# Performance work log

Hardware: AMD Instinct MI355X
Metric: run time of the kernel (lower is better)

Reference implementation:

```python
import jax, jax.numpy as jnp
import numpy as np

# --- quantization-format simulation helpers (numpy, used only in setup) ---
FP4_GRID = np.array([0.0, 0.5, 1.0, 1.5, 2.0, 3.0, 4.0, 6.0], np.float32)  # e2m1 magnitudes
FP4_MID = (FP4_GRID[:-1] + FP4_GRID[1:]) / 2.0
E4M3_MAX = 448.0


def _round_e4m3(x):
    """Round-to-nearest onto an fp8 e4m3-like grid (3 mantissa bits, clamp to 448)."""
    x = np.clip(x, -E4M3_MAX, E4M3_MAX)
    a = np.abs(x)
    e = np.clip(np.floor(np.log2(np.maximum(a, 1e-12))), -6, 8)
    step = np.exp2(e - 3)
    return (np.round(x / step) * step).astype(np.float32)


def _quant_fp4_mag(a):
    """Nearest e2m1 magnitude for non-negative a."""
    idx = np.searchsorted(FP4_MID, a)
    return FP4_GRID[idx]


def setup_inputs() -> dict:
    rng = np.random.default_rng(0)
    IN, OUT, P = 4096, 4096, 8
    k_fp8 = ((IN // P + 127) // 128) * 128   # 512
    k_fp4 = IN - k_fp8                       # 3584

    w = (rng.standard_normal((OUT, IN)) * 0.023).astype(np.float32)
    w4 = w[:, :k_fp4]
    w8 = w[:, k_fp4:]

    # --- NVFP4 quantization: per-128 fp32 outer scale, per-16 e4m3 inner scale ---
    b128 = w4.reshape(OUT, k_fp4 // 128, 128)
    os = np.maximum(np.abs(b128).max(-1) / (6.0 * E4M3_MAX), 1e-12).astype(np.float32)  # (OUT, k4/128)
    b16 = w4.reshape(OUT, k_fp4 // 128, 8, 16)
    is_q = _round_e4m3(np.abs(b16).max(-1) / 6.0 / os[..., None])  # (OUT, k4/128, 8)
    denom = np.maximum(is_q * os[..., None], 1e-12)
    q4 = np.sign(b16) * _quant_fp4_mag(np.abs(b16) / denom[..., None])
    w_q_fp4 = q4.reshape(OUT, k_fp4).astype(np.float32)
    w_is_fp4 = is_q.reshape(OUT, k_fp4 // 16).astype(np.float32)
    w_os_fp4 = os

    # --- fp8 quantization: per-32 e8m0 (power-of-2) scale ---
    b32 = w8.reshape(OUT, k_fp8 // 32, 32)
    amax = np.maximum(np.abs(b32).max(-1), 1e-12)
    s8 = np.exp2(np.ceil(np.log2(amax / E4M3_MAX))).astype(np.float32)
    w_q_fp8 = _round_e4m3(b32 / s8[..., None]).reshape(OUT, k_fp8)
    w_s_fp8 = s8

    # --- dequantized transposed weight buffer (as the module precomputes) ---
    w4_dq = w_q_fp4 * np.repeat(w_is_fp4, 16, 1) * np.repeat(w_os_fp4, 128, 1)
    w8_dq = w_q_fp8 * np.repeat(w_s_fp8, 32, 1)
    w_t = np.ascontiguousarray(np.concatenate([w4_dq, w8_dq], 1).T)  # (IN, OUT)

    x = rng.standard_normal((8192, IN)).astype(np.float32)
    return {
        "x": jnp.asarray(x),
        "w_q_fp4": jnp.asarray(w_q_fp4),
        "w_os_fp4": jnp.asarray(w_os_fp4),
        "w_is_fp4": jnp.asarray(w_is_fp4),
        "w_t": jnp.asarray(w_t),
        "w_q_fp8": jnp.asarray(w_q_fp8),
        "w_s_fp8": jnp.asarray(w_s_fp8),
    }


def reference(x, w_q_fp4, w_os_fp4, w_is_fp4, w_t, w_q_fp8, w_s_fp8):
    OUT = w_q_fp4.shape[0]
    k4 = w_q_fp4.shape[1]
    # fused dequant of fp4 partition: value * inner_scale(per 16) * outer_scale(per 128)
    w4 = (w_q_fp4.reshape(OUT, k4 // 16, 16) * w_is_fp4[..., None]).reshape(OUT, k4)
    w4 = (w4.reshape(OUT, k4 // 128, 128) * w_os_fp4[..., None]).reshape(OUT, k4)
    # dequant of fp8 partition: value * e8m0 scale (per 32)
    k8 = w_q_fp8.shape[1]
    w8 = (w_q_fp8.reshape(OUT, k8 // 32, 32) * w_s_fp8[..., None]).reshape(OUT, k8)
    W = jnp.concatenate([w4, w8], axis=1)  # (OUT, IN)
    return x @ W.T  # (tokens, OUT)
```

## Files before the change

kernel.cpp:

```cpp
#include <hip/hip_runtime.h>
#include <stdint.h>

#define K_DIM 4096
#define N_DIM 4096
#define KS_DIM (K_DIM / 32)
#define NT_DIM (N_DIM / 16)

typedef __attribute__((ext_vector_type(8))) short s16x8;
typedef __attribute__((ext_vector_type(4))) float f32x4;

static __device__ __forceinline__ unsigned short f32_to_bf16(float f) {
    union { float f; unsigned int u; } v; v.f = f;
    unsigned int u = v.u;
    u += 0x7FFFu + ((u >> 16) & 1u);
    return (unsigned short)(u >> 16);
}


extern "C" __global__ __launch_bounds__(256)
void pack_x_k(const float* __restrict__ in,
              unsigned short* __restrict__ out, int MT) {
    __shared__ __align__(16) unsigned short tile[16][1032];
    const int kc = blockIdx.x;
    const int mt = blockIdx.y;
    const int t = threadIdx.x;
#pragma unroll
    for (int r = 0; r < 16; ++r) {
        float4 v = *(const float4*)(in + (size_t)(mt * 16 + r) * K_DIM
                                    + kc * 1024 + t * 4);
        tile[r][t * 4 + 0] = f32_to_bf16(v.x);
        tile[r][t * 4 + 1] = f32_to_bf16(v.y);
        tile[r][t * 4 + 2] = f32_to_bf16(v.z);
        tile[r][t * 4 + 3] = f32_to_bf16(v.w);
    }
    __syncthreads();
#pragma unroll
    for (int i = 0; i < 8; ++i) {
        int chunk = i * 256 + t;
        int f = chunk >> 6, L = chunk & 63;
        int r = L & 15, q = L >> 4;
        s16x8 v = *(const s16x8*)&tile[r][f * 32 + q * 8];
        int ks = kc * 32 + f;
        *(s16x8*)(out + ((size_t)(ks * MT + mt) * 64 + L) * 8) = v;
    }
}

extern "C" __global__ void pack_w_k(const float* __restrict__ in,
                                    unsigned short* __restrict__ out) {
    __shared__ __align__(16) unsigned short tile[64][72];
    int n0 = blockIdx.x * 64, k0 = blockIdx.y * 64;
    int t = threadIdx.x;
    int tr = t >> 4, tc = (t & 15) * 4;
#pragma unroll
    for (int i = 0; i < 4; ++i) {
        int k = tr + i * 16;
        float4 v = *(const float4*)(in + (size_t)(k0 + k) * N_DIM + n0 + tc);
        tile[tc + 0][k] = f32_to_bf16(v.x);
        tile[tc + 1][k] = f32_to_bf16(v.y);
        tile[tc + 2][k] = f32_to_bf16(v.z);
        tile[tc + 3][k] = f32_to_bf16(v.w);
    }
    __syncthreads();
    int f = t >> 5, h = f >> 2, ntl = f & 3;
    int ks = blockIdx.y * 2 + h;
    int nt = blockIdx.x * 4 + ntl;
    unsigned short* dst = out + ((size_t)(ks * NT_DIM + nt) * 64) * 8;
#pragma unroll
    for (int u = 0; u < 2; ++u) {
        int c = (t & 31) * 2 + u;
        int r = c & 15, q = c >> 4;
        s16x8 o = *(const s16x8*)&tile[ntl * 16 + r][h * 32 + q * 8];
        *(s16x8*)(dst + (size_t)c * 8) = o;
    }
}

__device__ __forceinline__ void async_cp16(const unsigned short* g, unsigned short* l) {
    __builtin_amdgcn_global_load_lds(
        (const __attribute__((address_space(1))) unsigned int*)g,
        (__attribute__((address_space(3))) unsigned int*)l, 16, 0, 0);
}

#define SLOTS 4
#define SLOT_SHORTS (32 * 512)

__device__ __forceinline__ void sbar() {
    __builtin_amdgcn_sched_barrier(0);
    __builtin_amdgcn_s_barrier();
    __builtin_amdgcn_sched_barrier(0);
}

template <int VM>
__device__ __forceinline__ void wait_vm() {
    if constexpr (VM == 8)      asm volatile("s_waitcnt vmcnt(8)" ::: "memory");
    else if constexpr (VM == 4) asm volatile("s_waitcnt vmcnt(4)" ::: "memory");
    else if constexpr (VM == 0) asm volatile("s_waitcnt vmcnt(0)" ::: "memory");
    if constexpr (VM >= 0) __builtin_amdgcn_sched_barrier(0);
}

__device__ __forceinline__ void lgkm0() {
    asm volatile("s_waitcnt lgkmcnt(0)" ::: "memory");
    __builtin_amdgcn_sched_barrier(0);
}

#define BODY(T, VM, STAGE)                                                  \
  {                                                                         \
    const unsigned short* a = lds + ((T) & 3) * SLOT_SHORTS + aOff;         \
    const unsigned short* b = lds + ((T) & 3) * SLOT_SHORTS + bOff;         \
    unsigned short* d = lds + (((T) + 3) & 3) * SLOT_SHORTS + dsOff;        \
                                                     \
    s16x8 af[4], bf[4];                                                     \
    _Pragma("unroll")                                                       \
    for (int i = 0; i < 4; ++i) af[i] = *(const s16x8*)(a + i * 512);       \
    _Pragma("unroll")                                                       \
    for (int j = 0; j < 4; ++j) bf[j] = *(const s16x8*)(b + j * 512);       \
    if (STAGE) {                                                            \
      async_cp16(gstage + 0 * 512, d + 0 * 512);                            \
      async_cp16(gstage + 1 * 512, d + 1 * 512);                            \
    }                                                                       \
    sbar();                                                                 \
    lgkm0();                                                                \
    __builtin_amdgcn_s_setprio(1);                                          \
    _Pragma("unroll")                                                       \
    for (int i = 0; i < 4; ++i)                                             \
      _Pragma("unroll")                                                     \
      for (int j = 0; j < 4; ++j)                                           \
        acc[i][j] = __builtin_amdgcn_mfma_f32_16x16x32_bf16(                \
            af[i], bf[j], acc[i][j], 0, 0, 0);                              \
    __builtin_amdgcn_s_setprio(0);                                          \
                                                     \
    s16x8 ag[4];                                                            \
    _Pragma("unroll")                                                       \
    for (int i = 0; i < 4; ++i) ag[i] = *(const s16x8*)(a + (4 + i) * 512); \
    if (STAGE) {                                                            \
      async_cp16(gstage + 2 * 512, d + 2 * 512);                            \
      async_cp16(gstage + 3 * 512, d + 3 * 512);                            \
      gstage += strideS;                                                    \
    }                                                                       \
    wait_vm<VM>();                                                          \
    sbar();                                                                 \
    lgkm0();                                                                \
    __builtin_amdgcn_s_setprio(1);                                          \
    _Pragma("unroll")                                                       \
    for (int i = 0; i < 4; ++i)                                             \
      _Pragma("unroll")                                                     \
      for (int j = 0; j < 4; ++j)                                           \
        acc[4 + i][j] = __builtin_amdgcn_mfma_f32_16x16x32_bf16(            \
            ag[i], bf[j], acc[4 + i][j], 0, 0, 0);                          \
    __builtin_amdgcn_s_setprio(0);                                          \
  }

extern "C" __global__ __launch_bounds__(512, 2)
void gemm_pk(const unsigned short* __restrict__ Ap,
             const unsigned short* __restrict__ Bp,
             float* __restrict__ C, int M) {
    __shared__ __align__(16) unsigned short lds[SLOTS * SLOT_SHORTS];
    const int MT = M >> 4;
    const int tid = threadIdx.x;
    const int wave = tid >> 6, lane = tid & 63;

    const int nwg = gridDim.x;
    const int cpx = nwg >> 3;
    const int swz = (blockIdx.x & 7) * cpx + (blockIdx.x >> 3);
    const int bn = swz & (N_DIM / 256 - 1);
    const int bm = swz >> 4;

    const int wm2 = wave >> 2;
    const int wn4 = wave & 3;
    const int fr0 = (wave & 3) * 4;

    const unsigned short* gstage = wm2
        ? Bp + (((size_t)bn * 16 + fr0) * 64 + lane) * 8
        : Ap + (((size_t)bm * 16 + fr0) * 64 + lane) * 8;
    const size_t strideS = (size_t)(wm2 ? NT_DIM : MT) * 512;
    const int dsOff = (wm2 * 16 + fr0) * 512;

    const int aOff = (wm2 * 8) * 512 + lane * 8;
    const int bOff = (16 + wn4 * 4) * 512 + lane * 8;

    f32x4 acc[8][4] = {};

#pragma unroll
    for (int t = 0; t < SLOTS - 1; ++t) {
        unsigned short* d = lds + t * SLOT_SHORTS + dsOff;
#pragma unroll
        for (int fi = 0; fi < 4; ++fi)
            async_cp16(gstage + fi * 512, d + fi * 512);
        gstage += strideS;
    }
    wait_vm<8>();
    sbar();

    for (int t = 0; t < KS_DIM - 3; ++t)
        BODY(t, 8, true);
    BODY(KS_DIM - 3, 4, false);
    BODY(KS_DIM - 2, 0, false);
    BODY(KS_DIM - 1, -1, false);

    const size_t tileM = (size_t)bm * 256, tileN = (size_t)bn * 256;
#pragma unroll
    for (int i = 0; i < 8; ++i)
#pragma unroll
        for (int j = 0; j < 4; ++j) {
            size_t row = tileM + wm2 * 128 + i * 16 + (lane >> 4) * 4;
            size_t col = tileN + wn4 * 64 + j * 16 + (lane & 15);
#pragma unroll
            for (int r = 0; r < 4; ++r)
                C[(row + r) * N_DIM + col] = acc[i][j][r];
        }
}

extern "C" __global__ __launch_bounds__(256)
void gemm_f32_k(const float* __restrict__ X,
                const float* __restrict__ Wt,
                float* __restrict__ C, int M) {
    const int K = K_DIM, N = N_DIM;
    __shared__ __align__(16) unsigned short sA[128 * 32];
    __shared__ __align__(16) unsigned short sB[128 * 32];
    const int tid = threadIdx.x;
    const int wave = tid >> 6, lane = tid & 63;
    const int wm = (wave >> 1) * 64, wn = (wave & 1) * 64;
    const size_t tileM = (size_t)blockIdx.y * 128, tileN = (size_t)blockIdx.x * 128;
    const int frow = lane & 15, fcol = (lane >> 4) * 8;
    f32x4 acc[4][4] = {};
    for (int k0 = 0; k0 < K; k0 += 32) {
        __syncthreads();
#pragma unroll
        for (int it = 0; it < 4; ++it) {
            int idx = it * 256 + tid;
            int m = idx >> 3, c4 = (idx & 7) * 4;
            float4 v = *(const float4*)(X + (tileM + m) * (size_t)K + k0 + c4);
            sA[m * 32 + c4 + 0] = f32_to_bf16(v.x);
            sA[m * 32 + c4 + 1] = f32_to_bf16(v.y);
            sA[m * 32 + c4 + 2] = f32_to_bf16(v.z);
            sA[m * 32 + c4 + 3] = f32_to_bf16(v.w);
        }
#pragma unroll
        for (int it = 0; it < 16; ++it) {
            int idx = it * 256 + tid;
            int k = idx >> 7, n = idx & 127;
            float v = Wt[(size_t)(k0 + k) * N + tileN + n];
            sB[n * 32 + k] = f32_to_bf16(v);
        }
        __syncthreads();
        s16x8 af[4], bfr[4];
#pragma unroll
        for (int i = 0; i < 4; ++i)
            af[i] = *(const s16x8*)(sA + (wm + i * 16 + frow) * 32 + fcol);
#pragma unroll
        for (int j = 0; j < 4; ++j)
            bfr[j] = *(const s16x8*)(sB + (wn + j * 16 + frow) * 32 + fcol);
#pragma unroll
        for (int i = 0; i < 4; ++i)
#pragma unroll
            for (int j = 0; j < 4; ++j)
                acc[i][j] = __builtin_amdgcn_mfma_f32_16x16x32_bf16(
                    af[i], bfr[j], acc[i][j], 0, 0, 0);
    }
#pragma unroll
    for (int i = 0; i < 4; ++i)
#pragma unroll
        for (int j = 0; j < 4; ++j) {
            size_t row = tileM + wm + i * 16 + (lane >> 4) * 4;
            size_t col = tileN + wn + j * 16 + (lane & 15);
#pragma unroll
            for (int r = 0; r < 4; ++r)
                C[(row + r) * N + col] = acc[i][j][r];
        }
}

extern "C" void kernel_launch(void* const* d_in, const int* in_sizes, int n_in,
                              void* d_out, int out_size, void* d_ws, size_t ws_size,
                              hipStream_t stream) {
    const float* x   = (const float*)d_in[0];
    const float* w_t = (const float*)d_in[4];
    float* out = (float*)d_out;
    const int K = K_DIM, N = N_DIM;
    const int M = in_sizes[0] / K;
    const int MT = M / 16;
    const size_t need = (size_t)M * K * 2 + (size_t)N * K * 2;
    if (ws_size >= need && (M % 256) == 0) {
        unsigned short* ap = (unsigned short*)d_ws;
        unsigned short* bp = ap + (size_t)M * K;
        hipLaunchKernelGGL(pack_x_k, dim3(K / 1024, M / 16), dim3(256), 0, stream,
                           x, ap, MT);
        hipLaunchKernelGGL(pack_w_k, dim3(N / 64, K / 64), dim3(256), 0, stream,
                           w_t, bp);
        hipLaunchKernelGGL(gemm_pk, dim3((M / 256) * (N / 256)), dim3(512), 0,
                           stream, ap, bp, out, M);
    } else {
        hipLaunchKernelGGL(gemm_f32_k, dim3(N / 128, M / 128), dim3(256), 0, stream,
                           x, w_t, out, M);
    }
}
```

Before: 517.4 us.

## Fuse activation fp32-to-bf16 conversion into GEMM main loop via register staging

Drops the separate pack_x_k pass. The GEMM now loads fp32 activation rows straight into registers, converts them to bf16 in-loop, and writes them into the LDS slot one stage ahead. The weight operand still streams through async global-to-LDS copies. This avoids writing and re-reading a bf16 copy of x in HBM and one kernel launch. In exchange, every workgroup that shares an M tile re-reads and re-converts fp32 x, doubling A-side global traffic per tile, and the pipeline now needs extra registers and rebalanced vmcnt waits.

```diff
diff --git a/kernel.cpp b/kernel.cpp
--- a/kernel.cpp
+++ b/kernel.cpp
@@ -16,34 +16,15 @@
     return (unsigned short)(u >> 16);
 }
 
-
-extern "C" __global__ __launch_bounds__(256)
-void pack_x_k(const float* __restrict__ in,
-              unsigned short* __restrict__ out, int MT) {
-    __shared__ __align__(16) unsigned short tile[16][1032];
-    const int kc = blockIdx.x;
-    const int mt = blockIdx.y;
-    const int t = threadIdx.x;
-#pragma unroll
-    for (int r = 0; r < 16; ++r) {
-        float4 v = *(const float4*)(in + (size_t)(mt * 16 + r) * K_DIM
-                                    + kc * 1024 + t * 4);
-        tile[r][t * 4 + 0] = f32_to_bf16(v.x);
-        tile[r][t * 4 + 1] = f32_to_bf16(v.y);
-        tile[r][t * 4 + 2] = f32_to_bf16(v.z);
-        tile[r][t * 4 + 3] = f32_to_bf16(v.w);
-    }
-    __syncthreads();
-#pragma unroll
-    for (int i = 0; i < 8; ++i) {
-        int chunk = i * 256 + t;
-        int f = chunk >> 6, L = chunk & 63;
-        int r = L & 15, q = L >> 4;
-        s16x8 v = *(const s16x8*)&tile[r][f * 32 + q * 8];
-        int ks = kc * 32 + f;
-        *(s16x8*)(out + ((size_t)(ks * MT + mt) * 64 + L) * 8) = v;
-    }
-}
+static __device__ __forceinline__ s16x8 cvt8(float4 a, float4 b) {
+    s16x8 o;
+    o[0] = (short)f32_to_bf16(a.x); o[1] = (short)f32_to_bf16(a.y);
+    o[2] = (short)f32_to_bf16(a.z); o[3] = (short)f32_to_bf16(a.w);
+    o[4] = (short)f32_to_bf16(b.x); o[5] = (short)f32_to_bf16(b.y);
+    o[6] = (short)f32_to_bf16(b.z); o[7] = (short)f32_to_bf16(b.w);
+    return o;
+}
+
 
 extern "C" __global__ void pack_w_k(const float* __restrict__ in,
                                     unsigned short* __restrict__ out) {
@@ -92,7 +73,9 @@
 template <int VM>
 __device__ __forceinline__ void wait_vm() {
     if constexpr (VM == 8)      asm volatile("s_waitcnt vmcnt(8)" ::: "memory");
-    else if constexpr (VM == 4) asm volatile("s_waitcnt vmcnt(4)" ::: "memory");
+    else if constexpr (VM == 7) asm volatile("s_waitcnt vmcnt(7)" ::: "memory");
+    else if constexpr (VM == 6) asm volatile("s_waitcnt vmcnt(6)" ::: "memory");
+    else if constexpr (VM == 5) asm volatile("s_waitcnt vmcnt(5)" ::: "memory");
     else if constexpr (VM == 0) asm volatile("s_waitcnt vmcnt(0)" ::: "memory");
     if constexpr (VM >= 0) __builtin_amdgcn_sched_barrier(0);
 }
@@ -102,21 +85,23 @@
     __builtin_amdgcn_sched_barrier(0);
 }
 
-#define BODY(T, VM, STAGE)                                                  \
+#define BODY(T, RI, RC, VM, SA, SB, CW)                                     \
   {                                                                         \
     const unsigned short* a = lds + ((T) & 3) * SLOT_SHORTS + aOff;         \
     const unsigned short* b = lds + ((T) & 3) * SLOT_SHORTS + bOff;         \
-    unsigned short* d = lds + (((T) + 3) & 3) * SLOT_SHORTS + dsOff;        \
+    unsigned short* dB = lds + (((T) + 3) & 3) * SLOT_SHORTS + dsB;         \
                                                      \
     s16x8 af[4], bf[4];                                                     \
     _Pragma("unroll")                                                       \
     for (int i = 0; i < 4; ++i) af[i] = *(const s16x8*)(a + i * 512);       \
     _Pragma("unroll")                                                       \
     for (int j = 0; j < 4; ++j) bf[j] = *(const s16x8*)(b + j * 512);       \
-    if (STAGE) {                                                            \
-      async_cp16(gstage + 0 * 512, d + 0 * 512);                            \
-      async_cp16(gstage + 1 * 512, d + 1 * 512);                            \
+    if (SA) {                                                               \
+      RI[0] = *(const float4*)gA0;                                          \
+      RI[1] = *(const float4*)(gA0 + 4);                                    \
     }                                                                       \
+    __builtin_amdgcn_sched_barrier(0);                                      \
+    if (SB) async_cp16(gB, dB);                                             \
     sbar();                                                                 \
     lgkm0();                                                                \
     __builtin_amdgcn_s_setprio(1);                                          \
@@ -131,14 +116,25 @@
     s16x8 ag[4];                                                            \
     _Pragma("unroll")                                                       \
     for (int i = 0; i < 4; ++i) ag[i] = *(const s16x8*)(a + (4 + i) * 512); \
-    if (STAGE) {                                                            \
-      async_cp16(gstage + 2 * 512, d + 2 * 512);                            \
-      async_cp16(gstage + 3 * 512, d + 3 * 512);                            \
-      gstage += strideS;                                                    \
+    if (SA) {                                                               \
+      RI[2] = *(const float4*)gA1;                                          \
+      RI[3] = *(const float4*)(gA1 + 4);                                    \
+      gA0 += 32; gA1 += 32;                                                 \
     }                                                                       \
+    __builtin_amdgcn_sched_barrier(0);                                      \
+    if (SB) { async_cp16(gB + 512, dB + 512); gB += (size_t)NT_DIM * 512; } \
+    __builtin_amdgcn_sched_barrier(0);                                      \
     wait_vm<VM>();                                                          \
+    if (CW) {                                                               \
+      s16x8 o0 = cvt8(RC[0], RC[1]);                                        \
+      s16x8 o1 = cvt8(RC[2], RC[3]);                                        \
+      unsigned short* wv =                                                  \
+          lds + (((T) + 1) & 3) * SLOT_SHORTS + dsA + lane * 8;             \
+      *(s16x8*)wv = o0;                                                     \
+      *(s16x8*)(wv + 512) = o1;                                             \
+    }                                                                       \
+    lgkm0();   \
     sbar();                                                                 \
-    lgkm0();                                                                \
     __builtin_amdgcn_s_setprio(1);                                          \
     _Pragma("unroll")                                                       \
     for (int i = 0; i < 4; ++i)                                             \
@@ -150,11 +146,10 @@
   }
 
 extern "C" __global__ __launch_bounds__(512, 2)
-void gemm_pk(const unsigned short* __restrict__ Ap,
+void gemm_pk(const float* __restrict__ X,
              const unsigned short* __restrict__ Bp,
              float* __restrict__ C, int M) {
     __shared__ __align__(16) unsigned short lds[SLOTS * SLOT_SHORTS];
-    const int MT = M >> 4;
     const int tid = threadIdx.x;
     const int wave = tid >> 6, lane = tid & 63;
 
@@ -166,35 +161,57 @@
 
     const int wm2 = wave >> 2;
     const int wn4 = wave & 3;
-    const int fr0 = (wave & 3) * 4;
-
-    const unsigned short* gstage = wm2
-        ? Bp + (((size_t)bn * 16 + fr0) * 64 + lane) * 8
-        : Ap + (((size_t)bm * 16 + fr0) * 64 + lane) * 8;
-    const size_t strideS = (size_t)(wm2 ? NT_DIM : MT) * 512;
-    const int dsOff = (wm2 * 16 + fr0) * 512;
 
     const int aOff = (wm2 * 8) * 512 + lane * 8;
     const int bOff = (16 + wn4 * 4) * 512 + lane * 8;
 
+    const int dsA = (wave * 2) * 512;
+    const int dsB = (16 + wave * 2) * 512;
+    const float* gA0 = X + (size_t)(bm * 256 + wave * 32 + (lane & 15)) * K_DIM
+                         + ((lane >> 4) * 8);
+    const float* gA1 = gA0 + (size_t)16 * K_DIM;
+    const unsigned short* gB =
+        Bp + (((size_t)bn * 16 + wave * 2) * 64 + lane) * 8;
+
     f32x4 acc[8][4] = {};
-
-#pragma unroll
-    for (int t = 0; t < SLOTS - 1; ++t) {
-        unsigned short* d = lds + t * SLOT_SHORTS + dsOff;
-#pragma unroll
-        for (int fi = 0; fi < 4; ++fi)
-            async_cp16(gstage + fi * 512, d + fi * 512);
-        gstage += strideS;
-    }
+    float4 r0[4], r1[4];
+
+    r0[0] = *(const float4*)gA0; r0[1] = *(const float4*)(gA0 + 4);
+    r0[2] = *(const float4*)gA1; r0[3] = *(const float4*)(gA1 + 4);
+    gA0 += 32; gA1 += 32;
+    __builtin_amdgcn_sched_barrier(0);
+#pragma unroll
+    for (int tt = 0; tt < 3; ++tt) {
+        unsigned short* d = lds + tt * SLOT_SHORTS + dsB;
+        async_cp16(gB, d);
+        async_cp16(gB + 512, d + 512);
+        gB += (size_t)NT_DIM * 512;
+    }
+    __builtin_amdgcn_sched_barrier(0);
+    wait_vm<6>();
+    {
+        s16x8 o0 = cvt8(r0[0], r0[1]);
+        s16x8 o1 = cvt8(r0[2], r0[3]);
+        unsigned short* wv = lds + dsA + lane * 8;
+        *(s16x8*)wv = o0;
+        *(s16x8*)(wv + 512) = o1;
+    }
+    r1[0] = *(const float4*)gA0; r1[1] = *(const float4*)(gA0 + 4);
+    r1[2] = *(const float4*)gA1; r1[3] = *(const float4*)(gA1 + 4);
+    gA0 += 32; gA1 += 32;
+    __builtin_amdgcn_sched_barrier(0);
     wait_vm<8>();
+    lgkm0();
     sbar();
 
-    for (int t = 0; t < KS_DIM - 3; ++t)
-        BODY(t, 8, true);
-    BODY(KS_DIM - 3, 4, false);
-    BODY(KS_DIM - 2, 0, false);
-    BODY(KS_DIM - 1, -1, false);
+    BODY(0, r0, r1, 6, 1, 1, 1);
+    for (int t = 1; t < 125; t += 2) {
+        BODY(t,     r1, r0, 7, 1, 1, 1);
+        BODY(t + 1, r0, r1, 7, 1, 1, 1);
+    }
+    BODY(125, r1, r0, 5, 1, 0, 1);
+    BODY(126, r0, r1, 0, 0, 0, 1);
+    BODY(127, r1, r0, -1, 0, 0, 0);
 
     const size_t tileM = (size_t)bm * 256, tileN = (size_t)bn * 256;
 #pragma unroll
@@ -276,17 +293,13 @@
     float* out = (float*)d_out;
     const int K = K_DIM, N = N_DIM;
     const int M = in_sizes[0] / K;
-    const int MT = M / 16;
-    const size_t need = (size_t)M * K * 2 + (size_t)N * K * 2;
+    const size_t need = (size_t)N * K * 2;
     if (ws_size >= need && (M % 256) == 0) {
-        unsigned short* ap = (unsigned short*)d_ws;
-        unsigned short* bp = ap + (size_t)M * K;
-        hipLaunchKernelGGL(pack_x_k, dim3(K / 1024, M / 16), dim3(256), 0, stream,
-                           x, ap, MT);
+        unsigned short* bp = (unsigned short*)d_ws;
         hipLaunchKernelGGL(pack_w_k, dim3(N / 64, K / 64), dim3(256), 0, stream,
                            w_t, bp);
         hipLaunchKernelGGL(gemm_pk, dim3((M / 256) * (N / 256)), dim3(512), 0,
-                           stream, ap, bp, out, M);
+                           stream, x, bp, out, M);
     } else {
         hipLaunchKernelGGL(gemm_f32_k, dim3(N / 128, M / 128), dim3(256), 0, stream,
                            x, w_t, out, M);
```

New measurement: 722.3 us. +39.6%, slower.
